# Optimization experiments

Measured on AMD Instinct MI355X. Metric: run time of the kernel, lower is better.

Reference implementation:

```python
import jax, jax.numpy as jnp
import numpy as np

# pywt db4 decomposition low-pass filter
_DEC_LO = jnp.array([-0.010597401785069032, 0.0328830116668852, 0.030841381835560764,
                     -0.18703481171909309, -0.027983769416859854, 0.6308807679298589,
                     0.7148465705529157, 0.2303778133088965], dtype=jnp.float32)
_L = 8
_SIGN = jnp.where(jnp.arange(_L) % 2 == 0, -1.0, 1.0).astype(jnp.float32)
_DEC_HI = _SIGN * _DEC_LO[::-1]            # QMF: dec_hi[k] = (-1)^(k+1) dec_lo[L-1-k]
_REC_LO = _DEC_LO[::-1]
_REC_HI = _DEC_HI[::-1]
_LEVELS = 4


def _conv_valid(x, f):
    # x: [N, n]; true convolution (filter flipped), valid part
    k = f[::-1][None, None, :]
    return jax.lax.conv_general_dilated(x[:, None, :], k, (1,), 'VALID',
                                        dimension_numbers=('NCH', 'OIH', 'NCH'))[:, 0, :]


def _dwt(x):
    # one symmetric-mode DWT level; x: [N, n] -> (cA, cD) each [N, (n+L-1)//2]
    xp = jnp.pad(x, ((0, 0), (_L - 1, _L - 1)), mode='symmetric')
    return _conv_valid(xp, _DEC_LO)[:, 1::2], _conv_valid(xp, _DEC_HI)[:, 1::2]


def _idwt(a, d):
    # inverse DWT level; a,d: [N, m] -> [N, 2m-L+2]
    m = a.shape[-1]
    up_a = jnp.zeros((a.shape[0], 2 * m - 1), a.dtype).at[:, ::2].set(a)
    up_d = jnp.zeros((d.shape[0], 2 * m - 1), d.dtype).at[:, ::2].set(d)
    y = (_conv_valid(jnp.pad(up_a, ((0, 0), (_L - 1, _L - 1))), _REC_LO)
         + _conv_valid(jnp.pad(up_d, ((0, 0), (_L - 1, _L - 1))), _REC_HI))
    return y[:, _L - 2: y.shape[-1] - (_L - 2)]


def _wavelet_compress(x, level):
    # batched equivalent of the per-(b,c) pywt wavedec/threshold/waverec loop
    B, C, T = x.shape
    a = x.reshape(B * C, T)
    details = []
    for _ in range(_LEVELS):
        a, d = _dwt(a)
        details.append(d)
    thr = level * jnp.std(a, axis=-1, keepdims=True)  # np.std (ddof=0) of approx coeffs per row
    hard = lambda c: jnp.where(jnp.abs(c) < thr, jnp.zeros((), c.dtype), c)
    a = hard(a)
    for d in reversed(details):
        d = hard(d)
        if a.shape[-1] > d.shape[-1]:
            a = a[:, :d.shape[-1]]  # pywt waverec length alignment
        a = _idwt(a, d)
    if a.shape[-1] >= T:
        a = a[:, :T]
    else:
        a = jnp.pad(a, ((0, 0), (0, T - a.shape[-1])))
    return a.reshape(B, C, T)


def _spectral_distortion(x, key, freq_mask_prob=0.3, time_mask_prob=0.3):
    T = x.shape[-1]
    k1, k2, k3, k4 = jax.random.split(key, 4)
    X = jnp.fft.fft(x, axis=-1)
    mag, ph = jnp.abs(X), jnp.angle(X)
    idx = jnp.arange(T)
    fw = int(0.1 * T)
    f0 = jax.random.randint(k2, (), 0, T - fw)
    apply_f = jax.random.uniform(k1, ()) < freq_mask_prob
    fmask = apply_f & (idx >= f0) & (idx < f0 + fw)
    mag = mag * jnp.where(fmask, 0.1, 1.0).astype(mag.dtype)
    xd = jnp.fft.ifft(mag * jnp.exp(1j * ph), axis=-1).real.astype(x.dtype)
    tw = int(0.05 * T)
    t0 = jax.random.randint(k4, (), 0, T - tw)
    apply_t = jax.random.uniform(k3, ()) < time_mask_prob
    tmask = apply_t & (idx >= t0) & (idx < t0 + tw)
    return xd * jnp.where(tmask, 0.1, 1.0).astype(x.dtype)


def _add_noise(x, key, noise_std=0.02):
    # torch.std is unbiased -> ddof=1
    noise = jax.random.normal(key, x.shape, x.dtype) * noise_std * jnp.std(x, axis=-1, keepdims=True, ddof=1)
    return x + noise


def setup_inputs() -> dict:
    key = jax.random.key(0)
    x = jax.random.normal(key, (64, 64, 4096), dtype=jnp.float32)
    return {"x": x}


def reference(x):
    compression_level = 0.5  # fixed draw from compression_levels for determinism
    kd, kn, kcd, kcn = jax.random.split(jax.random.key(42), 4)
    compressed = _wavelet_compress(x, compression_level)
    distorted = _spectral_distortion(x, kd)
    noisy = _add_noise(x, kn)
    comb = _wavelet_compress(x, compression_level * 0.5)
    comb = _spectral_distortion(comb, kcd)
    comb = _add_noise(comb, kcn)
    # views: original, compressed, distorted, noisy, combined
    return (x, compressed, distorted, noisy, comb)
```

## Files before the change

### kernel.cpp

```cpp
#include <hip/hip_runtime.h>
#include <stdint.h>

#define T_LEN 4096
#define N_ROWS 4096
#define N_ELEM (4096u * 4096u)
#define PD(i) ((i) + ((i) >> 5))

__constant__ float c_DEC_LO[8] = {
  -0.010597401785069032f, 0.0328830116668852f, 0.030841381835560764f,
  -0.18703481171909309f, -0.027983769416859854f, 0.6308807679298589f,
   0.7148465705529157f, 0.2303778133088965f };
__constant__ float c_DEC_HI[8] = {
  -0.2303778133088965f, 0.7148465705529157f, -0.6308807679298589f,
  -0.027983769416859854f, 0.18703481171909309f, 0.030841381835560764f,
  -0.0328830116668852f, -0.010597401785069032f };

#define RL0 0.2303778133088965f
#define RL1 0.7148465705529157f
#define RL2 0.6308807679298589f
#define RL3 (-0.027983769416859854f)
#define RL4 (-0.18703481171909309f)
#define RL5 0.030841381835560764f
#define RL6 0.0328830116668852f
#define RL7 (-0.010597401785069032f)
#define RH0 (-0.010597401785069032f)
#define RH1 (-0.0328830116668852f)
#define RH2 0.030841381835560764f
#define RH3 0.18703481171909309f
#define RH4 (-0.027983769416859854f)
#define RH5 (-0.6308807679298589f)
#define RH6 0.7148465705529157f
#define RH7 (-0.2303778133088965f)

__host__ __device__ __forceinline__ uint32_t rotl32(uint32_t v, int r) {
  return (v << r) | (v >> (32 - r));
}

__host__ __device__ __forceinline__ void tf2x32(uint32_t k0, uint32_t k1,
                                                uint32_t c0, uint32_t c1,
                                                uint32_t& o0, uint32_t& o1) {
  uint32_t ks2 = k0 ^ k1 ^ 0x1BD11BDAu;
  uint32_t x0 = c0 + k0;
  uint32_t x1 = c1 + k1;
#define TFR(r) { x0 += x1; x1 = rotl32(x1, r); x1 ^= x0; }
  TFR(13) TFR(15) TFR(26) TFR(6)
  x0 += k1;  x1 += ks2 + 1u;
  TFR(17) TFR(29) TFR(16) TFR(24)
  x0 += ks2; x1 += k0 + 2u;
  TFR(13) TFR(15) TFR(26) TFR(6)
  x0 += k0;  x1 += k1 + 3u;
  TFR(17) TFR(29) TFR(16) TFR(24)
  x0 += k1;  x1 += ks2 + 4u;
  TFR(13) TFR(15) TFR(26) TFR(6)
  x0 += ks2; x1 += k0 + 5u;
#undef TFR
  o0 = x0; o1 = x1;
}

__host__ __device__ __forceinline__ uint32_t jbits_scalar(uint32_t kx, uint32_t ky) {
  uint32_t a, b; tf2x32(kx, ky, 0u, 0u, a, b);
  return a ^ b;
}

__device__ __forceinline__ uint32_t jbits_elem(uint32_t kx, uint32_t ky, uint32_t i) {
  uint32_t a, b; tf2x32(kx, ky, 0u, i, a, b); return a ^ b;
}

__host__ __device__ __forceinline__ float junif_scalar(uint32_t kx, uint32_t ky) {
  union { uint32_t u; float f; } cv;
  cv.u = (jbits_scalar(kx, ky) >> 9) | 0x3f800000u;
  return cv.f - 1.0f;
}

__host__ __device__ __forceinline__ void jsplit2(uint32_t kx, uint32_t ky, uint32_t* o) {
  tf2x32(kx, ky, 0u, 0u, o[0], o[1]);
  tf2x32(kx, ky, 0u, 1u, o[2], o[3]);
}

__host__ __device__ __forceinline__ void jsplit4(uint32_t kx, uint32_t ky, uint32_t* o) {
  tf2x32(kx, ky, 0u, 0u, o[0], o[1]);
  tf2x32(kx, ky, 0u, 1u, o[2], o[3]);
  tf2x32(kx, ky, 0u, 2u, o[4], o[5]);
  tf2x32(kx, ky, 0u, 3u, o[6], o[7]);
}

__host__ __device__ __forceinline__ int jrandint(uint32_t kx, uint32_t ky, uint32_t span) {
  uint32_t c[4];
  jsplit2(kx, ky, c);
  uint32_t hi = jbits_scalar(c[0], c[1]);
  uint32_t lo = jbits_scalar(c[2], c[3]);
  uint32_t mult = 65536u % span;
  mult = (mult * mult) % span;
  uint32_t off = ((hi % span) * mult + (lo % span)) % span;
  return (int)off;
}

__host__ __device__ void distort_params(uint32_t kx, uint32_t ky,
                                        int* f0, int* af, int* t0, int* at) {
  uint32_t q[8];
  jsplit4(kx, ky, q);
  *af = junif_scalar(q[0], q[1]) < 0.3f;
  *f0 = jrandint(q[2], q[3], 3687u);
  *at = junif_scalar(q[4], q[5]) < 0.3f;
  *t0 = jrandint(q[6], q[7], 3892u);
}

__device__ __forceinline__ float erfinv32(float x) {
  float w = -log1pf(-x * x);
  float p;
  if (w < 5.0f) {
    w = w - 2.5f;
    p = 2.81022636e-08f;
    p = fmaf(p, w, 3.43273939e-07f);
    p = fmaf(p, w, -3.5233877e-06f);
    p = fmaf(p, w, -4.39150654e-06f);
    p = fmaf(p, w, 0.00021858087f);
    p = fmaf(p, w, -0.00125372503f);
    p = fmaf(p, w, -0.00417768164f);
    p = fmaf(p, w, 0.246640727f);
    p = fmaf(p, w, 1.50140941f);
  } else {
    w = sqrtf(w) - 3.0f;
    p = -0.000200214257f;
    p = fmaf(p, w, 0.000100950558f);
    p = fmaf(p, w, 0.00134934322f);
    p = fmaf(p, w, -0.00367342844f);
    p = fmaf(p, w, 0.00573950773f);
    p = fmaf(p, w, -0.0076224613f);
    p = fmaf(p, w, 0.00943887047f);
    p = fmaf(p, w, 1.00167406f);
    p = fmaf(p, w, 2.83297682f);
  }
  return p * x;
}

__device__ __forceinline__ float jax_normal_from_bits(uint32_t bits) {
  union { uint32_t u; float f; } cv;
  cv.u = (bits >> 9) | 0x3f800000u;
  float f = cv.f - 1.0f;
  const float lo = -0.99999994f;
  float u = __fadd_rn(__fmul_rn(f, 2.0f), lo);
  u = fmaxf(lo, u);
  return 1.41421356f * erfinv32(u);
}

__device__ __forceinline__ float tree8(const float* p) {
  return __fadd_rn(
      __fadd_rn(__fadd_rn(p[0], p[1]), __fadd_rn(p[2], p[3])),
      __fadd_rn(__fadd_rn(p[4], p[5]), __fadd_rn(p[6], p[7])));
}

__device__ __forceinline__ void dwt_one(const float* a, int n, int i,
                                        float* oA, float* oD) {
  int base = 2 * i - 6;
  float pa[8], pd[8];
  #pragma unroll
  for (int j = 0; j < 8; ++j) {
    int q = base + j;
    q = (q < 0) ? (-q - 1) : ((q >= n) ? (2 * n - 1 - q) : q);
    float xv = a[q];
    pa[j] = __fmul_rn(c_DEC_LO[7 - j], xv);
    pd[j] = __fmul_rn(c_DEC_HI[7 - j], xv);
  }
  *oA = tree8(pa); *oD = tree8(pd);
}

__device__ void dwt_step(const float* a, int n, float* oa, float* od,
                         int nOut, int tid) {
  int iHi = (n - 2) >> 1;
  int nPair = nOut >> 1;
  for (int u = tid; u < nPair; u += 256) {
    int i0 = 2 * u;
    if (u >= 2 && (i0 + 1) <= iHi) {
      int base = 2 * i0 - 6;
      float x[10];
      #pragma unroll
      for (int j = 0; j < 10; ++j) x[j] = a[base + j];
      float p0[8], p1[8], q0[8], q1[8];
      #pragma unroll
      for (int j = 0; j < 8; ++j) {
        p0[j] = __fmul_rn(c_DEC_LO[7 - j], x[j]);
        q0[j] = __fmul_rn(c_DEC_HI[7 - j], x[j]);
        p1[j] = __fmul_rn(c_DEC_LO[7 - j], x[j + 2]);
        q1[j] = __fmul_rn(c_DEC_HI[7 - j], x[j + 2]);
      }
      *reinterpret_cast<float2*>(&oa[i0]) = make_float2(tree8(p0), tree8(p1));
      *reinterpret_cast<float2*>(&od[i0]) = make_float2(tree8(q0), tree8(q1));
    } else {
      float a0, d0, a1, d1;
      dwt_one(a, n, i0, &a0, &d0);
      dwt_one(a, n, i0 + 1, &a1, &d1);
      oa[i0] = a0; od[i0] = d0;
      oa[i0 + 1] = a1; od[i0 + 1] = d1;
    }
  }
  for (int i = 2 * nPair + tid; i < nOut; i += 256) {
    float av, dv;
    dwt_one(a, n, i, &av, &dv);
    oa[i] = av; od[i] = dv;
  }
}

__device__ __forceinline__ void idwt_pair_vals(const float* __restrict__ a,
                                               const float* __restrict__ d,
                                               int h, float thr, bool trA,
                                               float* ev, float* ov) {
  float a0 = a[h], a1 = a[h + 1], a2 = a[h + 2], a3 = a[h + 3];
  if (trA) {
    a0 = (fabsf(a0) < thr) ? 0.f : a0;
    a1 = (fabsf(a1) < thr) ? 0.f : a1;
    a2 = (fabsf(a2) < thr) ? 0.f : a2;
    a3 = (fabsf(a3) < thr) ? 0.f : a3;
  }
  float d0 = d[h], d1 = d[h + 1], d2 = d[h + 2], d3 = d[h + 3];
  d0 = (fabsf(d0) < thr) ? 0.f : d0;
  d1 = (fabsf(d1) < thr) ? 0.f : d1;
  d2 = (fabsf(d2) < thr) ? 0.f : d2;
  d3 = (fabsf(d3) < thr) ? 0.f : d3;
  float saE = __fadd_rn(__fadd_rn(__fmul_rn(RL6, a0), __fmul_rn(RL4, a1)),
                        __fadd_rn(__fmul_rn(RL2, a2), __fmul_rn(RL0, a3)));
  float sdE = __fadd_rn(__fadd_rn(__fmul_rn(RH6, d0), __fmul_rn(RH4, d1)),
                        __fadd_rn(__fmul_rn(RH2, d2), __fmul_rn(RH0, d3)));
  float saO = __fadd_rn(__fadd_rn(__fmul_rn(RL7, a0), __fmul_rn(RL5, a1)),
                        __fadd_rn(__fmul_rn(RL3, a2), __fmul_rn(RL1, a3)));
  float sdO = __fadd_rn(__fadd_rn(__fmul_rn(RH7, d0), __fmul_rn(RH5, d1)),
                        __fadd_rn(__fmul_rn(RH3, d2), __fmul_rn(RH1, d3)));
  *ev = __fadd_rn(saE, sdE);
  *ov = __fadd_rn(saO, sdO);
}

__device__ void idwt_step(const float* __restrict__ a, const float* __restrict__ d,
                          float* __restrict__ out, int nOut, float thr,
                          bool trA, int tid) {
  int nPair = nOut >> 1;
  for (int h = tid; h < nPair; h += 256) {
    float ev, ov;
    idwt_pair_vals(a, d, h, thr, trA, &ev, &ov);
    *reinterpret_cast<float2*>(&out[2 * h]) = make_float2(ev, ov);
  }
  if (nOut & 1) {
    int h = nPair;
    if (tid == (h & 255)) {
      float ev, ov;
      idwt_pair_vals(a, d, h, thr, trA, &ev, &ov);
      out[2 * h] = ev;
    }
  }
}

__device__ void idwt_last_store(const float* __restrict__ a, const float* __restrict__ d,
                                float thr, int tid, float* __restrict__ dstRow) {
  #pragma unroll
  for (int k = 0; k < 8; ++k) {
    int h = tid + (k << 8);
    float ev, ov;
    idwt_pair_vals(a, d, h, thr, false, &ev, &ov);
    *reinterpret_cast<float2*>(&dstRow[2 * h]) = make_float2(ev, ov);
  }
}

__device__ void idwt_last_reg(const float* __restrict__ a, const float* __restrict__ d,
                              float thr, int tid, float* w) {
  #pragma unroll
  for (int k = 0; k < 8; ++k) {
    int h = tid + (k << 8);
    idwt_pair_vals(a, d, h, thr, false, &w[2 * k], &w[2 * k + 1]);
  }
}

__device__ void np_pw262_partials(const float* src, float* pbuf, int tid) {
  if (tid < 24) {
    int blk = tid >> 3, k = tid & 7;
    const float* base = src + (blk == 0 ? 0 : (blk == 1 ? 128 : 192));
    int iters = (blk == 0 ? 16 : 8);
    float r = base[k];
    for (int it = 1; it < iters; ++it) r = __fadd_rn(r, base[8 * it + k]);
    pbuf[tid] = r;
  }
}

__device__ float np_pw262_combine(const float* src, const float* pbuf) {
  float b0 = tree8(pbuf + 0);
  float b1 = tree8(pbuf + 8);
  float b2 = tree8(pbuf + 16);
  for (int i = 256; i < 262; ++i) b2 = __fadd_rn(b2, src[i]);
  return __fadd_rn(b0, __fadd_rn(b1, b2));
}

__global__ __launch_bounds__(256)
void wavelet_kernel(const float* __restrict__ x, float* __restrict__ out0,
                    float* __restrict__ out1, float* __restrict__ out4,
                    int fuse, int at_c, int t0_c, uint32_t kcx, uint32_t kcy) {
  extern __shared__ float smem[];
  float* A  = smem;
  float* B  = smem + 4096;
  float* D1 = smem + 6148;
  float* D2 = smem + 8200;
  float* D3 = smem + 9230;
  float* D4 = smem + 9748;
  float* SC = smem + 10010;
  float* Bp = B + 512;
  const int row = blockIdx.x, tid = threadIdx.x;
  const float4* s4 = reinterpret_cast<const float4*>(x + (size_t)row * T_LEN);
  float4* o04 = reinterpret_cast<float4*>(out0 + (size_t)row * T_LEN);
  #pragma unroll
  for (int k = 0; k < 4; ++k) {
    float4 v = s4[tid + (k << 8)];
    *reinterpret_cast<float4*>(&A[4 * (tid + (k << 8))]) = v;
    o04[tid + (k << 8)] = v;
  }
  __syncthreads();
  dwt_step(A, 4096, B, D1, 2051, tid); __syncthreads();
  dwt_step(B, 2051, A, D2, 1029, tid); __syncthreads();
  dwt_step(A, 1029, B, D3, 518, tid);  __syncthreads();
  dwt_step(B, 518, A, D4, 262, tid);   __syncthreads();

  np_pw262_partials(A, Bp, tid);
  __syncthreads();
  if (tid == 0) SC[0] = np_pw262_combine(A, Bp) / 262.0f;
  __syncthreads();
  float mu = SC[0];
  for (int i = tid; i < 262; i += 256) {
    float dv = __fsub_rn(A[i], mu);
    B[i] = __fmul_rn(dv, dv);
  }
  __syncthreads();
  np_pw262_partials(B, Bp, tid);
  __syncthreads();
  if (tid == 0) SC[1] = __fsqrt_rn(np_pw262_combine(B, Bp) / 262.0f);
  __syncthreads();
  float sigma = SC[1];

  float ra0 = A[tid];
  float ra1 = (tid < 6) ? A[256 + tid] : 0.f;

  {
    float thr = __fmul_rn(0.5f, sigma);
    idwt_step(A, D4, B, 518, thr, true, tid);   __syncthreads();
    idwt_step(B, D3, A, 1029, thr, false, tid); __syncthreads();
    idwt_step(A, D2, B, 2051, thr, false, tid); __syncthreads();
    idwt_last_store(B, D1, thr, tid, out1 + (size_t)row * T_LEN);
    __syncthreads();
  }
  A[tid] = ra0;
  if (tid < 6) A[256 + tid] = ra1;
  __syncthreads();

  float thr = __fmul_rn(0.25f, sigma);
  idwt_step(A, D4, B, 518, thr, true, tid);   __syncthreads();
  idwt_step(B, D3, A, 1029, thr, false, tid); __syncthreads();
  idwt_step(A, D2, B, 2051, thr, false, tid); __syncthreads();

  float* dstRow = out4 + (size_t)row * T_LEN;
  if (!fuse) {
    idwt_last_store(B, D1, thr, tid, dstRow);
    return;
  }

  float w[16];
  idwt_last_reg(B, D1, thr, tid, w);
  if (at_c) {
    #pragma unroll
    for (int k = 0; k < 8; ++k) {
      #pragma unroll
      for (int c = 0; c < 2; ++c) {
        int col = 2 * (tid + (k << 8)) + c;
        if (col >= t0_c && col < t0_c + 204) w[2 * k + c] *= 0.1f;
      }
    }
  }
  __syncthreads();
  float* red = B;
  float acc = 0.f;
  #pragma unroll
  for (int i = 0; i < 16; ++i) acc += w[i];
  red[tid] = acc; __syncthreads();
  for (int o = 128; o > 0; o >>= 1) { if (tid < o) red[tid] += red[tid + o]; __syncthreads(); }
  float nmu = red[0] * (1.0f / 4096.0f);
  __syncthreads();
  acc = 0.f;
  #pragma unroll
  for (int i = 0; i < 16; ++i) { float dv = w[i] - nmu; acc += dv * dv; }
  red[tid] = acc; __syncthreads();
  for (int o = 128; o > 0; o >>= 1) { if (tid < o) red[tid] += red[tid + o]; __syncthreads(); }
  float nsig = sqrtf(red[0] / 4095.0f);

  #pragma unroll
  for (int k = 0; k < 8; ++k) {
    int h = tid + (k << 8);
    float o2v[2];
    #pragma unroll
    for (int c = 0; c < 2; ++c) {
      uint32_t col = (uint32_t)(2 * h + c);
      uint32_t idx = ((uint32_t)row << 12) + col;
      float z = jax_normal_from_bits(jbits_elem(kcx, kcy, idx));
      o2v[c] = w[2 * k + c] + __fmul_rn(__fmul_rn(z, 0.02f), nsig);
    }
    *reinterpret_cast<float2*>(&dstRow[2 * h]) = make_float2(o2v[0], o2v[1]);
  }
}

__constant__ int c_STW_OFF[6] = {0, 1024, 1280, 1344, 1360, 1364};

__global__ __launch_bounds__(256)
void distort_noise_kernel(const float* __restrict__ src, float* __restrict__ dst_d,
                          float* __restrict__ dst_n,
                          int af, int f0, int at, int t0, int nod, int wd,
                          uint32_t kx, uint32_t ky) {
  extern __shared__ float smem[];
  float* RE = smem;
  float* IM = smem + 4224;
  float2* STW = (float2*)(smem + 8448);
  const int row = blockIdx.x, tid = threadIdx.x;

  const float4* s4 = reinterpret_cast<const float4*>(src + (size_t)row * T_LEN);
  float4 v4[4];
  #pragma unroll
  for (int k = 0; k < 4; ++k) v4[k] = s4[tid + (k << 8)];

  float w[16];
  if (af) {
    for (int t = tid; t < 1365; t += 256) {
      int s, j;
      if (t < 1024) { s = 0; j = t; }
      else if (t < 1280) { s = 1; j = t - 1024; }
      else if (t < 1344) { s = 2; j = t - 1280; }
      else if (t < 1360) { s = 3; j = t - 1344; }
      else if (t < 1364) { s = 4; j = t - 1360; }
      else { s = 5; j = 0; }
      int e = j << (2 * s);
      float ang = (float)e * (-1.5339807878856412e-3f);
      float sn, cs;
      __sincosf(ang, &sn, &cs);
      STW[t] = make_float2(cs, sn);
    }
    #pragma unroll
    for (int k = 0; k < 4; ++k) {
      int p = 4 * (tid + (k << 8));
      RE[PD(p + 0)] = v4[k].x; IM[PD(p + 0)] = 0.f;
      RE[PD(p + 1)] = v4[k].y; IM[PD(p + 1)] = 0.f;
      RE[PD(p + 2)] = v4[k].z; IM[PD(p + 2)] = 0.f;
      RE[PD(p + 3)] = v4[k].w; IM[PD(p + 3)] = 0.f;
    }
    __syncthreads();
    for (int s = 0; s < 6; ++s) {
      int Lsh = 12 - 2 * s, Qsh = Lsh - 2, Qm = (1 << Qsh) - 1, off = c_STW_OFF[s];
      for (int b = tid; b < 1024; b += 256) {
        int j = b & Qm, g = b >> Qsh;
        int i0 = (g << Lsh) + j;
        int i1 = i0 + (1 << Qsh), i2 = i1 + (1 << Qsh), i3 = i2 + (1 << Qsh);
        float x0r = RE[PD(i0)], x0i = IM[PD(i0)];
        float x1r = RE[PD(i1)], x1i = IM[PD(i1)];
        float x2r = RE[PD(i2)], x2i = IM[PD(i2)];
        float x3r = RE[PD(i3)], x3i = IM[PD(i3)];
        float t0r = x0r + x2r, t0i = x0i + x2i;
        float t1r = x0r - x2r, t1i = x0i - x2i;
        float t2r = x1r + x3r, t2i = x1i + x3i;
        float t3r = x1r - x3r, t3i = x1i - x3i;
        float2 w1 = STW[off + j];
        float c1 = w1.x, s1 = w1.y;
        float c2 = c1 * c1 - s1 * s1, s2 = 2.f * c1 * s1;
        float c3 = c1 * c2 - s1 * s2, s3 = c1 * s2 + s1 * c2;
        RE[PD(i0)] = t0r + t2r; IM[PD(i0)] = t0i + t2i;
        float u1r = t1r + t3i, u1i = t1i - t3r;
        RE[PD(i1)] = u1r * c1 - u1i * s1; IM[PD(i1)] = u1r * s1 + u1i * c1;
        float u2r = t0r - t2r, u2i = t0i - t2i;
        RE[PD(i2)] = u2r * c2 - u2i * s2; IM[PD(i2)] = u2r * s2 + u2i * c2;
        float u3r = t1r - t3i, u3i = t1i + t3r;
        RE[PD(i3)] = u3r * c3 - u3i * s3; IM[PD(i3)] = u3r * s3 + u3i * c3;
      }
      __syncthreads();
    }
    for (int p = tid; p < 4096; p += 256) {
      uint32_t rb = __brev((uint32_t)p) >> 20;
      int kk = (int)(((rb & 0x555u) << 1) | ((rb >> 1) & 0x555u));
      if (kk >= f0 && kk < f0 + 409) { RE[PD(p)] *= 0.1f; IM[PD(p)] *= 0.1f; }
    }
    __syncthreads();
    for (int s = 5; s >= 0; --s) {
      int Lsh = 12 - 2 * s, Qsh = Lsh - 2, Qm = (1 << Qsh) - 1, off = c_STW_OFF[s];
      for (int b = tid; b < 1024; b += 256) {
        int j = b & Qm, g = b >> Qsh;
        int i0 = (g << Lsh) + j;
        int i1 = i0 + (1 << Qsh), i2 = i1 + (1 << Qsh), i3 = i2 + (1 << Qsh);
        float y0r = RE[PD(i0)], y0i = IM[PD(i0)];
        float y1r = RE[PD(i1)], y1i = IM[PD(i1)];
        float y2r = RE[PD(i2)], y2i = IM[PD(i2)];
        float y3r = RE[PD(i3)], y3i = IM[PD(i3)];
        float2 w1 = STW[off + j];
        float c1 = w1.x, s1 = -w1.y;
        float c2 = c1 * c1 - s1 * s1, s2 = 2.f * c1 * s1;
        float c3 = c1 * c2 - s1 * s2, s3 = c1 * s2 + s1 * c2;
        float z1r = y1r * c1 - y1i * s1, z1i = y1r * s1 + y1i * c1;
        float z2r = y2r * c2 - y2i * s2, z2i = y2r * s2 + y2i * c2;
        float z3r = y3r * c3 - y3i * s3, z3i = y3r * s3 + y3i * c3;
        float u0r = y0r + z2r, u0i = y0i + z2i;
        float u2r = y0r - z2r, u2i = y0i - z2i;
        float u1r = z1r + z3r, u1i = z1i + z3i;
        float u3r = z3i - z1i, u3i = z1r - z3r;
        RE[PD(i0)] = u0r + u1r; IM[PD(i0)] = u0i + u1i;
        RE[PD(i1)] = u2r + u3r; IM[PD(i1)] = u2i + u3i;
        RE[PD(i2)] = u0r - u1r; IM[PD(i2)] = u0i - u1i;
        RE[PD(i3)] = u2r - u3r; IM[PD(i3)] = u2i - u3i;
      }
      __syncthreads();
    }
    #pragma unroll
    for (int k = 0; k < 4; ++k) {
      int p = 4 * (tid + (k << 8));
      w[4 * k + 0] = RE[PD(p + 0)] * (1.0f / 4096.0f);
      w[4 * k + 1] = RE[PD(p + 1)] * (1.0f / 4096.0f);
      w[4 * k + 2] = RE[PD(p + 2)] * (1.0f / 4096.0f);
      w[4 * k + 3] = RE[PD(p + 3)] * (1.0f / 4096.0f);
    }
    __syncthreads();
  } else {
    #pragma unroll
    for (int k = 0; k < 4; ++k) {
      w[4 * k + 0] = v4[k].x; w[4 * k + 1] = v4[k].y;
      w[4 * k + 2] = v4[k].z; w[4 * k + 3] = v4[k].w;
    }
  }
  if (at) {
    #pragma unroll
    for (int i = 0; i < 16; ++i) {
      int col = 4 * (tid + ((i >> 2) << 8)) + (i & 3);
      if (col >= t0 && col < t0 + 204) w[i] *= 0.1f;
    }
  }
  if (wd) {
    float4* d4 = reinterpret_cast<float4*>(dst_d + (size_t)row * T_LEN);
    #pragma unroll
    for (int k = 0; k < 4; ++k)
      d4[tid + (k << 8)] = make_float4(w[4 * k], w[4 * k + 1], w[4 * k + 2], w[4 * k + 3]);
  }

  float nv[16];
  #pragma unroll
  for (int i = 0; i < 16; ++i) {
    float q;
    if (nod) q = w[i];
    else {
      float4 vv = v4[i >> 2];
      q = (i & 3) == 0 ? vv.x : (i & 3) == 1 ? vv.y : (i & 3) == 2 ? vv.z : vv.w;
    }
    nv[i] = q;
  }
  float* red = smem;
  float acc = 0.f;
  #pragma unroll
  for (int i = 0; i < 16; ++i) acc += nv[i];
  red[tid] = acc; __syncthreads();
  for (int o = 128; o > 0; o >>= 1) { if (tid < o) red[tid] += red[tid + o]; __syncthreads(); }
  float mu = red[0] * (1.0f / 4096.0f);
  __syncthreads();
  acc = 0.f;
  #pragma unroll
  for (int i = 0; i < 16; ++i) { float dv = nv[i] - mu; acc += dv * dv; }
  red[tid] = acc; __syncthreads();
  for (int o = 128; o > 0; o >>= 1) { if (tid < o) red[tid] += red[tid + o]; __syncthreads(); }
  float sigma = sqrtf(red[0] / 4095.0f);

  float4* n4 = reinterpret_cast<float4*>(dst_n + (size_t)row * T_LEN);
  #pragma unroll
  for (int k = 0; k < 4; ++k) {
    float o[4];
    #pragma unroll
    for (int c = 0; c < 4; ++c) {
      uint32_t col = (uint32_t)(4 * (tid + (k << 8)) + c);
      uint32_t idx = ((uint32_t)row << 12) + col;
      float z = jax_normal_from_bits(jbits_elem(kx, ky, idx));
      o[c] = nv[4 * k + c] + __fmul_rn(__fmul_rn(z, 0.02f), sigma);
    }
    n4[tid + (k << 8)] = make_float4(o[0], o[1], o[2], o[3]);
  }
}

extern "C" void kernel_launch(void* const* d_in, const int* in_sizes, int n_in,
                              void* d_out, int out_size, void* d_ws, size_t ws_size,
                              hipStream_t stream) {
  const float* x = (const float*)d_in[0];
  float* out = (float*)d_out;
  float* o0 = out;
  float* o1 = out + (size_t)N_ELEM;
  float* o2 = out + 2 * (size_t)N_ELEM;
  float* o3 = out + 3 * (size_t)N_ELEM;
  float* o4 = out + 4 * (size_t)N_ELEM;

  uint32_t r[8];
  jsplit4(0u, 42u, r);
  int f0d, afd, t0d, atd, f0c, afc, t0c, atc;
  distort_params(r[0], r[1], &f0d, &afd, &t0d, &atd);
  distort_params(r[4], r[5], &f0c, &afc, &t0c, &atc);

  const size_t WAVE_LDS = 10012u * 4u;
  const size_t FFT_LDS  = 11178u * 4u;

  hipLaunchKernelGGL(wavelet_kernel, dim3(N_ROWS), dim3(256), WAVE_LDS, stream,
                     x, o0, o1, o4, afc ? 0 : 1, atc, t0c, r[6], r[7]);
  hipLaunchKernelGGL(distort_noise_kernel, dim3(N_ROWS), dim3(256),
                     afd ? FFT_LDS : 1024, stream,
                     x, o2, o3, afd, f0d, atd, t0d, 0, 1, r[2], r[3]);
  if (afc) {
    hipLaunchKernelGGL(distort_noise_kernel, dim3(N_ROWS), dim3(256), FFT_LDS, stream,
                       o4, o4, o4, 1, f0c, atc, t0c, 1, 0, r[6], r[7]);
  }
}
```

Measured before the change: 329.1 us.

## Use real-input FFT via half-length complex FFT with spectral untangling

```diff
diff --git a/kernel.cpp b/kernel.cpp
--- a/kernel.cpp
+++ b/kernel.cpp
@@ -400,52 +400,66 @@
   }
 }
 
-__constant__ int c_STW_OFF[6] = {0, 1024, 1280, 1344, 1360, 1364};
-
-__global__ __launch_bounds__(256)
-void distort_noise_kernel(const float* __restrict__ src, float* __restrict__ dst_d,
-                          float* __restrict__ dst_n,
-                          int af, int f0, int at, int t0, int nod, int wd,
-                          uint32_t kx, uint32_t ky) {
-  extern __shared__ float smem[];
+__constant__ int c_STW2_OFF[5] = {0, 512, 640, 672, 680};
+
+__device__ __forceinline__ int rev2048(int k) {
+  return ((k & 3) << 9) | (((k >> 2) & 3) << 7) | (((k >> 4) & 3) << 5)
+       | (((k >> 6) & 3) << 3) | (((k >> 8) & 3) << 1) | (k >> 10);
+}
+
+__device__ __forceinline__ float maskP(int K, int f0) {
+  float m1 = (K >= f0 && K < f0 + 409) ? 0.1f : 1.0f;
+  int K2 = (4096 - K) & 4095;
+  float m2 = (K2 >= f0 && K2 < f0 + 409) ? 0.1f : 1.0f;
+  return 0.5f * (m1 + m2);
+}
+
+__device__ __forceinline__ void retangle_one(int k, int f0,
+    float zkr, float zki, float zmr, float zmi, float* outr, float* outi) {
+  float xer = 0.5f * (zkr + zmr), xei = 0.5f * (zki - zmi);
+  float xor_ = 0.5f * (zki + zmi), xoi = 0.5f * (zmr - zkr);
+  float sn, cs;
+  __sincosf((float)k * (-1.5339807878856412e-3f), &sn, &cs);
+  float wxr = xor_ * cs - xoi * sn, wxi = xor_ * sn + xoi * cs;
+  float X1r = xer + wxr, X1i = xei + wxi;
+  float X2r = xer - wxr, X2i = xei - wxi;
+  float m1 = maskP(k, f0), m2 = maskP(k + 2048, f0);
+  X1r *= m1; X1i *= m1; X2r *= m2; X2i *= m2;
+  float yer = 0.5f * (X1r + X2r), yei = 0.5f * (X1i + X2i);
+  float dr = 0.5f * (X1r - X2r), di = 0.5f * (X1i - X2i);
+  float yor = dr * cs + di * sn, yoi = di * cs - dr * sn;
+  *outr = yer - yoi; *outi = yei + yor;
+}
+
+__device__ void distort_core(float* smem, const float4* v4, float* w,
+                             int af, int f0, int at, int t0, int tid) {
   float* RE = smem;
-  float* IM = smem + 4224;
-  float2* STW = (float2*)(smem + 8448);
-  const int row = blockIdx.x, tid = threadIdx.x;
-
-  const float4* s4 = reinterpret_cast<const float4*>(src + (size_t)row * T_LEN);
-  float4 v4[4];
-  #pragma unroll
-  for (int k = 0; k < 4; ++k) v4[k] = s4[tid + (k << 8)];
-
-  float w[16];
+  float* IM = smem + 2112;
+  float2* STW = (float2*)(smem + 4224);
   if (af) {
-    for (int t = tid; t < 1365; t += 256) {
+    for (int t = tid; t < 682; t += 256) {
       int s, j;
-      if (t < 1024) { s = 0; j = t; }
-      else if (t < 1280) { s = 1; j = t - 1024; }
-      else if (t < 1344) { s = 2; j = t - 1280; }
-      else if (t < 1360) { s = 3; j = t - 1344; }
-      else if (t < 1364) { s = 4; j = t - 1360; }
-      else { s = 5; j = 0; }
+      if (t < 512) { s = 0; j = t; }
+      else if (t < 640) { s = 1; j = t - 512; }
+      else if (t < 672) { s = 2; j = t - 640; }
+      else if (t < 680) { s = 3; j = t - 672; }
+      else { s = 4; j = t - 680; }
       int e = j << (2 * s);
-      float ang = (float)e * (-1.5339807878856412e-3f);
+      float ang = (float)e * (-3.0679615757712823e-3f);
       float sn, cs;
       __sincosf(ang, &sn, &cs);
       STW[t] = make_float2(cs, sn);
     }
     #pragma unroll
     for (int k = 0; k < 4; ++k) {
-      int p = 4 * (tid + (k << 8));
-      RE[PD(p + 0)] = v4[k].x; IM[PD(p + 0)] = 0.f;
-      RE[PD(p + 1)] = v4[k].y; IM[PD(p + 1)] = 0.f;
-      RE[PD(p + 2)] = v4[k].z; IM[PD(p + 2)] = 0.f;
-      RE[PD(p + 3)] = v4[k].w; IM[PD(p + 3)] = 0.f;
+      int n = 2 * (tid + (k << 8));
+      RE[PD(n)]     = v4[k].x; IM[PD(n)]     = v4[k].y;
+      RE[PD(n + 1)] = v4[k].z; IM[PD(n + 1)] = v4[k].w;
     }
     __syncthreads();
-    for (int s = 0; s < 6; ++s) {
-      int Lsh = 12 - 2 * s, Qsh = Lsh - 2, Qm = (1 << Qsh) - 1, off = c_STW_OFF[s];
-      for (int b = tid; b < 1024; b += 256) {
+    for (int s = 0; s < 5; ++s) {
+      int Lsh = 11 - 2 * s, Qsh = Lsh - 2, Qm = (1 << Qsh) - 1, off = c_STW2_OFF[s];
+      for (int b = tid; b < 512; b += 256) {
         int j = b & Qm, g = b >> Qsh;
         int i0 = (g << Lsh) + j;
         int i1 = i0 + (1 << Qsh), i2 = i1 + (1 << Qsh), i3 = i2 + (1 << Qsh);
@@ -471,15 +485,52 @@
       }
       __syncthreads();
     }
-    for (int p = tid; p < 4096; p += 256) {
-      uint32_t rb = __brev((uint32_t)p) >> 20;
-      int kk = (int)(((rb & 0x555u) << 1) | ((rb >> 1) & 0x555u));
-      if (kk >= f0 && kk < f0 + 409) { RE[PD(p)] *= 0.1f; IM[PD(p)] *= 0.1f; }
+    for (int m = tid; m < 1024; m += 256) {
+      int i0 = 2 * m, i1 = 2 * m + 1;
+      float ar = RE[PD(i0)], ai = IM[PD(i0)];
+      float br = RE[PD(i1)], bi = IM[PD(i1)];
+      RE[PD(i0)] = ar + br; IM[PD(i0)] = ai + bi;
+      RE[PD(i1)] = ar - br; IM[PD(i1)] = ai - bi;
     }
     __syncthreads();
-    for (int s = 5; s >= 0; --s) {
-      int Lsh = 12 - 2 * s, Qsh = Lsh - 2, Qm = (1 << Qsh) - 1, off = c_STW_OFF[s];
-      for (int b = tid; b < 1024; b += 256) {
+    for (int k0 = tid; k0 < 1024; k0 += 256) {
+      if (k0 == 0) {
+        {
+          int pk = PD(rev2048(0));
+          float zr = RE[pk], zi = IM[pk], orr, oi;
+          retangle_one(0, f0, zr, zi, zr, zi, &orr, &oi);
+          RE[pk] = orr; IM[pk] = oi;
+        }
+        {
+          int pk = PD(rev2048(1024));
+          float zr = RE[pk], zi = IM[pk], orr, oi;
+          retangle_one(1024, f0, zr, zi, zr, zi, &orr, &oi);
+          RE[pk] = orr; IM[pk] = oi;
+        }
+      } else {
+        int m = 2048 - k0;
+        int pk = PD(rev2048(k0)), pm = PD(rev2048(m));
+        float zkr = RE[pk], zki = IM[pk];
+        float zmr = RE[pm], zmi = IM[pm];
+        float akr, aki, amr, ami;
+        retangle_one(k0, f0, zkr, zki, zmr, zmi, &akr, &aki);
+        retangle_one(m, f0, zmr, zmi, zkr, zki, &amr, &ami);
+        RE[pk] = akr; IM[pk] = aki;
+        RE[pm] = amr; IM[pm] = ami;
+      }
+    }
+    __syncthreads();
+    for (int m = tid; m < 1024; m += 256) {
+      int i0 = 2 * m, i1 = 2 * m + 1;
+      float ar = RE[PD(i0)], ai = IM[PD(i0)];
+      float br = RE[PD(i1)], bi = IM[PD(i1)];
+      RE[PD(i0)] = ar + br; IM[PD(i0)] = ai + bi;
+      RE[PD(i1)] = ar - br; IM[PD(i1)] = ai - bi;
+    }
+    __syncthreads();
+    for (int s = 4; s >= 0; --s) {
+      int Lsh = 11 - 2 * s, Qsh = Lsh - 2, Qm = (1 << Qsh) - 1, off = c_STW2_OFF[s];
+      for (int b = tid; b < 512; b += 256) {
         int j = b & Qm, g = b >> Qsh;
         int i0 = (g << Lsh) + j;
         int i1 = i0 + (1 << Qsh), i2 = i1 + (1 << Qsh), i3 = i2 + (1 << Qsh);
@@ -507,11 +558,11 @@
     }
     #pragma unroll
     for (int k = 0; k < 4; ++k) {
-      int p = 4 * (tid + (k << 8));
-      w[4 * k + 0] = RE[PD(p + 0)] * (1.0f / 4096.0f);
-      w[4 * k + 1] = RE[PD(p + 1)] * (1.0f / 4096.0f);
-      w[4 * k + 2] = RE[PD(p + 2)] * (1.0f / 4096.0f);
-      w[4 * k + 3] = RE[PD(p + 3)] * (1.0f / 4096.0f);
+      int n = 2 * (tid + (k << 8));
+      w[4 * k + 0] = RE[PD(n)]     * (1.0f / 2048.0f);
+      w[4 * k + 1] = IM[PD(n)]     * (1.0f / 2048.0f);
+      w[4 * k + 2] = RE[PD(n + 1)] * (1.0f / 2048.0f);
+      w[4 * k + 3] = IM[PD(n + 1)] * (1.0f / 2048.0f);
     }
     __syncthreads();
   } else {
@@ -528,6 +579,24 @@
       if (col >= t0 && col < t0 + 204) w[i] *= 0.1f;
     }
   }
+}
+
+__global__ __launch_bounds__(256)
+void distort_noise_kernel(const float* __restrict__ src, float* __restrict__ dst_d,
+                          float* __restrict__ dst_n,
+                          int af, int f0, int at, int t0, int nod, int wd,
+                          uint32_t kx, uint32_t ky) {
+  extern __shared__ float smem[];
+  const int row = blockIdx.x, tid = threadIdx.x;
+
+  const float4* s4 = reinterpret_cast<const float4*>(src + (size_t)row * T_LEN);
+  float4 v4[4];
+  #pragma unroll
+  for (int k = 0; k < 4; ++k) v4[k] = s4[tid + (k << 8)];
+
+  float w[16];
+  distort_core(smem, v4, w, af, f0, at, t0, tid);
+
   if (wd) {
     float4* d4 = reinterpret_cast<float4*>(dst_d + (size_t)row * T_LEN);
     #pragma unroll
@@ -594,7 +663,7 @@
   distort_params(r[4], r[5], &f0c, &afc, &t0c, &atc);
 
   const size_t WAVE_LDS = 10012u * 4u;
-  const size_t FFT_LDS  = 11178u * 4u;
+  const size_t FFT_LDS  = 5588u * 4u;
 
   hipLaunchKernelGGL(wavelet_kernel, dim3(N_ROWS), dim3(256), WAVE_LDS, stream,
                      x, o0, o1, o4, afc ? 0 : 1, atc, t0c, r[6], r[7]);
```

New measurement: 279.9 us. -15.0%, faster.
